# Kernel optimization log

Measured on AMD Instinct MI355X. Metric: run time of the kernel, lower is better.

The kernel has to match this reference:

```python
import jax, jax.numpy as jnp
import numpy as np

N_NODES = 50000


def _sage_conv(x, src, dst, Wl, bl, Wr):
    # PyG SAGEConv (mean aggr): out = lin_l(mean_{j in N(i)} x_j) + lin_r(x_i)
    msgs = x[src]                                              # [E, F]
    agg = jax.ops.segment_sum(msgs, dst, num_segments=N_NODES)  # [N, F]
    cnt = jax.ops.segment_sum(jnp.ones((dst.shape[0],), x.dtype), dst,
                              num_segments=N_NODES)
    mean = agg / jnp.maximum(cnt, 1.0)[:, None]
    return mean @ Wl + bl + x @ Wr


def setup_inputs() -> dict:
    key = jax.random.key(0)
    ks = jax.random.split(key, 12)
    in_c, hid_c, out_c = 128, 128, 64
    E, P = 800000, 200000
    s = lambda k, shp: jax.random.normal(k, shp, dtype=jnp.float32) * (1.0 / np.sqrt(shp[0]))
    return {
        "x": jax.random.normal(ks[0], (N_NODES, in_c), dtype=jnp.float32),
        "edge_index": jax.random.randint(ks[1], (2, E), 0, N_NODES),
        "edge_pairs": jax.random.randint(ks[2], (2, P), 0, N_NODES),
        "W1l": s(ks[3], (in_c, hid_c)),
        "b1": jnp.zeros((hid_c,), jnp.float32),
        "W1r": s(ks[4], (in_c, hid_c)),
        "W2l": s(ks[5], (hid_c, out_c)),
        "b2": jnp.zeros((out_c,), jnp.float32),
        "W2r": s(ks[6], (hid_c, out_c)),
        "Wlin": s(ks[7], (2 * out_c, 1)),
        "blin": jnp.zeros((1,), jnp.float32),
    }


def reference(x, edge_index, edge_pairs, W1l, b1, W1r, W2l, b2, W2r, Wlin, blin):
    src, dst = edge_index[0], edge_index[1]
    h = jax.nn.relu(_sage_conv(x, src, dst, W1l, b1, W1r))
    z = _sage_conv(h, src, dst, W2l, b2, W2r)                 # [N, out_c]
    ps, pd = edge_pairs[0], edge_pairs[1]
    hcat = jnp.concatenate([z[ps], z[pd]], axis=1)            # [P, 2*out_c]
    logits = hcat @ Wlin + blin                               # [P, 1]
    return jax.nn.sigmoid(logits).reshape(-1)
```

## Files before the change

### kernel.cpp

```cpp
#include <hip/hip_runtime.h>
#include <math.h>


typedef __attribute__((ext_vector_type(8))) short bf16x8;
typedef __attribute__((ext_vector_type(4))) float f32x4;
typedef unsigned int uint32;
typedef unsigned short ushort16;

#define MAXBUCK 784
#define NHB 512
#define SLABB 2048

__device__ __forceinline__ ushort16 f2bf(float f) {
    uint32 u = __float_as_uint(f);
    uint32 r = u + 0x7FFFu + ((u >> 16) & 1u);
    return (ushort16)(r >> 16);
}


__global__ __launch_bounds__(256)
void prep_kernel(const float* __restrict__ x, uint32* __restrict__ xh, long long n4,
                 const float* __restrict__ W1l, const float* __restrict__ W1r,
                 ushort16* __restrict__ W1t,
                 const float* __restrict__ W2l, const float* __restrict__ W2r,
                 const float* __restrict__ Wlin, const float* __restrict__ b2,
                 float* __restrict__ fw, float* __restrict__ fc,
                 const int* __restrict__ dst, int* __restrict__ hcnt, int E,
                 int nbx, int nbw1) {
    __shared__ int lh[MAXBUCK];
    int b = blockIdx.x;
    int t = threadIdx.x;
    if (b < nbx) {
        long long i = (long long)b * 256 + t;
        if (i < n4) {
            float4 v = ((const float4*)x)[i];
            uint2 o;
            o.x = (uint32)f2bf(v.x) | ((uint32)f2bf(v.y) << 16);
            o.y = (uint32)f2bf(v.z) | ((uint32)f2bf(v.w) << 16);
            ((uint2*)xh)[i] = o;
        }
    } else if (b < nbx + nbw1) {
        int idx = (b - nbx) * 256 + t;
        int n = idx >> 8, k = idx & 255;
        float v = (k < 128) ? W1l[k * 128 + n] : W1r[(k - 128) * 128 + n];
        W1t[idx ^ ((n & 7) << 3)] = f2bf(v);
    } else if (b == nbx + nbw1) {
        if (t < 128) {
            float a = 0.f, c = 0.f;
            for (int l = 0; l < 64; ++l) {
                float w = W2l[t * 64 + l];
                a += w * Wlin[l];
                c += w * Wlin[64 + l];
            }
            fw[t] = a; fw[128 + t] = c;
        } else {
            int k = t - 128;
            float a = 0.f, c = 0.f;
            for (int l = 0; l < 64; ++l) {
                float w = W2r[k * 64 + l];
                a += w * Wlin[l];
                c += w * Wlin[64 + l];
            }
            fw[256 + k] = a; fw[384 + k] = c;
        }
        if (t == 0) { float s = 0.f; for (int l = 0; l < 64; ++l) s += b2[l] * Wlin[l];      fc[0] = s; }
        if (t == 1) { float s = 0.f; for (int l = 0; l < 64; ++l) s += b2[l] * Wlin[64 + l]; fc[1] = s; }
    } else {
        int hb = b - nbx - nbw1 - 1;
        for (int i = t; i < MAXBUCK; i += 256) lh[i] = 0;
        __syncthreads();
        int per = (E + NHB - 1) / NHB;
        int e0 = hb * per, e1 = min(e0 + per, E);
        for (int e = e0 + t; e < e1; e += 256) atomicAdd(&lh[dst[e] >> 6], 1);
        __syncthreads();
        for (int i = t; i < MAXBUCK; i += 256)
            hcnt[hb * MAXBUCK + i] = lh[i];
    }
}


__global__ __launch_bounds__(256)
void offs_kernel(const int* __restrict__ hcnt, int* __restrict__ boff,
                 int* __restrict__ tot) {
    int k = blockIdx.x * 4 + (threadIdx.x >> 6);
    int lane = threadIdx.x & 63;
    if (k >= MAXBUCK) return;
    int carry = 0;
    #pragma unroll
    for (int c = 0; c < NHB / 64; ++c) {
        int hb = c * 64 + lane;
        int v = hcnt[hb * MAXBUCK + k];
        int s = v;
        #pragma unroll
        for (int off = 1; off < 64; off <<= 1) {
            int u = __shfl_up(s, off, 64);
            if (lane >= off) s += u;
        }
        boff[hb * MAXBUCK + k] = carry + s - v;
        carry += __shfl(s, 63, 64);
    }
    if (lane == 0) tot[k] = carry;
}


__global__ __launch_bounds__(256)
void scatter_kernel(const int* __restrict__ src, const int* __restrict__ dst,
                    const int* __restrict__ boff,
                    uint32* __restrict__ recs, int E) {
    __shared__ int lh[MAXBUCK];
    __shared__ int lb[MAXBUCK];
    int t = threadIdx.x;
    int hb = blockIdx.x;
    int per = (E + NHB - 1) / NHB;
    int e0 = hb * per, e1 = min(e0 + per, E);
    for (int i = t; i < MAXBUCK; i += 256) {
        lh[i] = 0;
        lb[i] = i * SLABB + boff[hb * MAXBUCK + i];
    }
    __syncthreads();
    for (int e = e0 + t; e < e1; e += 256) {
        int d = dst[e];
        int bk = d >> 6;
        int r = atomicAdd(&lh[bk], 1);
        int p = lb[bk] + r;
        if (p < (bk + 1) * SLABB)
            recs[p] = (uint32)src[e] | ((uint32)(d & 63) << 16);
    }
}


__global__ __launch_bounds__(1024)
void sortagg_kernel(const uint32* __restrict__ xh,
                    const uint32* __restrict__ recs, const int* __restrict__ tot,
                    int2* __restrict__ rowse, ushort16* __restrict__ esrc_g,
                    uint32* __restrict__ meanh, int N) {
    __shared__ int lh[64];
    __shared__ int st_[64];
    __shared__ unsigned short es[SLABB];
    int b = blockIdx.x;
    int t = threadIdx.x;
    int s0 = b * SLABB;
    int cntb = tot[b]; if (cntb > SLABB) cntb = SLABB;
    int s1 = s0 + cntb;
    if (t < 64) lh[t] = 0;
    __syncthreads();
    for (int i = s0 + t; i < s1; i += 1024)
        atomicAdd(&lh[recs[i] >> 16], 1);
    __syncthreads();
    if (t < 64) {
        int v = lh[t];
        int incl = v;
        #pragma unroll
        for (int off = 1; off < 64; off <<= 1) {
            int u = __shfl_up(incl, off, 64);
            if (t >= off) incl += u;
        }
        int excl = incl - v;
        int node = b * 64 + t;
        if (node < N) rowse[node] = make_int2(s0 + excl, v);
        st_[t] = excl;
        lh[t] = excl;
    }
    __syncthreads();
    for (int i = s0 + t; i < s1; i += 1024) {
        uint32 r = recs[i];
        int pos = atomicAdd(&lh[r >> 16], 1);
        unsigned short sv = (unsigned short)(r & 0xFFFFu);
        es[pos] = sv;
        ((unsigned short*)esrc_g)[s0 + pos] = sv;
    }
    __syncthreads();

    int wave = t >> 6, lane = t & 63;
    int q = lane >> 4;
    int w = lane & 15;
    for (int rr = 0; rr < 4; ++rr) {
        int n = wave * 4 + rr;
        int node = b * 64 + n;
        if (node >= N) break;
        int e0 = st_[n], e1 = lh[n];
        if (e0 == e1) {
            if (q == 0) ((uint4*)meanh)[(size_t)node * 16 + w] = make_uint4(0u, 0u, 0u, 0u);
            continue;
        }
        float acc[8] = {};
        for (int k = e0; k < e1; k += 16) {
            int idx[4]; float msk[4];
            #pragma unroll
            for (int j = 0; j < 4; ++j) {
                int e = k + q * 4 + j;
                int valid = e < e1;
                idx[j] = es[valid ? e : e0];
                msk[j] = valid ? 1.f : 0.f;
            }
            #pragma unroll
            for (int j = 0; j < 4; ++j) {
                uint4 v = ((const uint4*)xh)[(size_t)idx[j] * 16 + w];
                acc[0] += __uint_as_float(v.x << 16) * msk[j];
                acc[1] += __uint_as_float(v.x & 0xFFFF0000u) * msk[j];
                acc[2] += __uint_as_float(v.y << 16) * msk[j];
                acc[3] += __uint_as_float(v.y & 0xFFFF0000u) * msk[j];
                acc[4] += __uint_as_float(v.z << 16) * msk[j];
                acc[5] += __uint_as_float(v.z & 0xFFFF0000u) * msk[j];
                acc[6] += __uint_as_float(v.w << 16) * msk[j];
                acc[7] += __uint_as_float(v.w & 0xFFFF0000u) * msk[j];
            }
        }
        #pragma unroll
        for (int i = 0; i < 8; ++i) {
            acc[i] += __shfl_xor(acc[i], 16, 64);
            acc[i] += __shfl_xor(acc[i], 32, 64);
        }
        if (q == 0) {
            float inv = 1.0f / (float)(e1 - e0);
            uint4 o;
            o.x = (uint32)f2bf(acc[0] * inv) | ((uint32)f2bf(acc[1] * inv) << 16);
            o.y = (uint32)f2bf(acc[2] * inv) | ((uint32)f2bf(acc[3] * inv) << 16);
            o.z = (uint32)f2bf(acc[4] * inv) | ((uint32)f2bf(acc[5] * inv) << 16);
            o.w = (uint32)f2bf(acc[6] * inv) | ((uint32)f2bf(acc[7] * inv) << 16);
            ((uint4*)meanh)[(size_t)node * 16 + w] = o;
        }
    }
}


__global__ __launch_bounds__(256)
void gemm1_mfma_kernel(const ushort16* __restrict__ meanh,
                       const ushort16* __restrict__ xh,
                       const ushort16* __restrict__ W1t,
                       const float* __restrict__ b1,
                       const float* __restrict__ fw,
                       float2* __restrict__ pab, float2* __restrict__ quv, int N) {
    __shared__ uint4 w1s[4096];
    for (int u = threadIdx.x; u < 4096; u += 256)
        w1s[u] = ((const uint4*)W1t)[u];
    __syncthreads();
    int wave = threadIdx.x >> 6;
    int lane = threadIdx.x & 63;
    int m = lane & 15;
    int quad = lane >> 4;
    int row0 = blockIdx.x * 128 + wave * 32;
    int ar0 = row0 + m;      if (ar0 > N - 1) ar0 = N - 1;
    int ar1 = row0 + 16 + m; if (ar1 > N - 1) ar1 = N - 1;
    const char* wbase = (const char*)w1s;
    f32x4 acc[2][8];
    #pragma unroll
    for (int h = 0; h < 2; ++h)
        #pragma unroll
        for (int c = 0; c < 8; ++c) acc[h][c] = (f32x4){0.f, 0.f, 0.f, 0.f};
    #pragma unroll
    for (int ks = 0; ks < 8; ++ks) {
        int k0 = ks * 32;
        const ushort16* Ab = (ks < 4) ? meanh : xh;
        bf16x8 a0 = *(const bf16x8*)(Ab + (size_t)ar0 * 128 + (k0 & 127) + quad * 8);
        bf16x8 a1 = *(const bf16x8*)(Ab + (size_t)ar1 * 128 + (k0 & 127) + quad * 8);
        #pragma unroll
        for (int c = 0; c < 8; ++c) {
            int boff_ = (((c * 16 + m) << 9) + ((k0 + quad * 8) << 1)) ^ ((m & 7) << 4);
            bf16x8 bfr = *(const bf16x8*)(wbase + boff_);
            acc[0][c] = __builtin_amdgcn_mfma_f32_16x16x32_bf16(a0, bfr, acc[0][c], 0, 0, 0);
            acc[1][c] = __builtin_amdgcn_mfma_f32_16x16x32_bf16(a1, bfr, acc[1][c], 0, 0, 0);
        }
    }
    float da[2][4] = {}, dc[2][4] = {}, db[2][4] = {}, dd[2][4] = {};
    #pragma unroll
    for (int c = 0; c < 8; ++c) {
        int col = c * 16 + m;
        float bias = b1[col];
        float wa = fw[col], wc = fw[128 + col], wb = fw[256 + col], wd = fw[384 + col];
        #pragma unroll
        for (int h = 0; h < 2; ++h) {
            #pragma unroll
            for (int r = 0; r < 4; ++r) {
                float v = fmaxf(acc[h][c][r] + bias, 0.f);
                da[h][r] += v * wa; dc[h][r] += v * wc;
                db[h][r] += v * wb; dd[h][r] += v * wd;
            }
        }
    }
    #pragma unroll
    for (int h = 0; h < 2; ++h) {
        #pragma unroll
        for (int r = 0; r < 4; ++r) {
            #pragma unroll
            for (int msk = 1; msk < 16; msk <<= 1) {
                da[h][r] += __shfl_xor(da[h][r], msk, 64);
                dc[h][r] += __shfl_xor(dc[h][r], msk, 64);
                db[h][r] += __shfl_xor(db[h][r], msk, 64);
                dd[h][r] += __shfl_xor(dd[h][r], msk, 64);
            }
        }
    }
    if (m == 0) {
        #pragma unroll
        for (int h = 0; h < 2; ++h) {
            #pragma unroll
            for (int r = 0; r < 4; ++r) {
                int grow = row0 + h * 16 + quad * 4 + r;
                if (grow < N) {
                    pab[grow] = make_float2(da[h][r], dc[h][r]);
                    quv[grow] = make_float2(db[h][r], dd[h][r]);
                }
            }
        }
    }
}


__global__ __launch_bounds__(256)
void agg_link_kernel(const float2* __restrict__ pab,
                     const float2* __restrict__ quv,
                     const int2* __restrict__ rowse,
                     const ushort16* __restrict__ esrc,
                     const float* __restrict__ fc,
                     float* __restrict__ za, float* __restrict__ zb, int N) {
    int gi = blockIdx.x * blockDim.x + threadIdx.x;
    int i = gi >> 2;
    int q = gi & 3;
    if (i >= N) return;
    int2 se = rowse[i];
    int s0 = se.x, s1 = se.x + se.y;
    float a0 = 0.f, c0 = 0.f, a1 = 0.f, c1 = 0.f;
    for (int k = s0 + q; k < s1; k += 8) {
        int kB = k + 4;
        int vB = kB < s1;
        int idxA = esrc[k];
        int idxB = esrc[vB ? kB : k];
        float2 pA = pab[idxA];
        float2 pB = pab[idxB];
        float mB = vB ? 1.f : 0.f;
        a0 += pA.x; c0 += pA.y;
        a1 += pB.x * mB; c1 += pB.y * mB;
    }
    float spa = a0 + a1, spc = c0 + c1;
    spa += __shfl_xor(spa, 1, 64); spa += __shfl_xor(spa, 2, 64);
    spc += __shfl_xor(spc, 1, 64); spc += __shfl_xor(spc, 2, 64);
    if (q == 0) {
        float inv = (se.y > 0) ? 1.0f / (float)se.y : 0.f;
        float2 qv = quv[i];
        za[i] = spa * inv + qv.x + fc[0];
        zb[i] = spc * inv + qv.y + fc[1];
    }
}


__global__ void link_kernel(const float* __restrict__ za, const float* __restrict__ zb,
                            const int* __restrict__ ps, const int* __restrict__ pd,
                            const float* __restrict__ blin,
                            float* __restrict__ out, int P) {
    int p = blockIdx.x * blockDim.x + threadIdx.x;
    if (p >= P) return;
    float logit = za[ps[p]] + zb[pd[p]] + blin[0];
    out[p] = 1.0f / (1.0f + expf(-logit));
}


extern "C" void kernel_launch(void* const* d_in, const int* in_sizes, int n_in,
                              void* d_out, int out_size, void* d_ws, size_t ws_size,
                              hipStream_t stream) {
    const float* x          = (const float*)d_in[0];
    const int*   edge_index = (const int*)d_in[1];
    const int*   edge_pairs = (const int*)d_in[2];
    const float* W1l        = (const float*)d_in[3];
    const float* b1         = (const float*)d_in[4];
    const float* W1r        = (const float*)d_in[5];
    const float* W2l        = (const float*)d_in[6];
    const float* b2         = (const float*)d_in[7];
    const float* W2r        = (const float*)d_in[8];
    const float* Wlin       = (const float*)d_in[9];
    const float* blin       = (const float*)d_in[10];
    float* out = (float*)d_out;

    const int N = in_sizes[0] / 128;
    const int E = in_sizes[1] / 2;
    const int P = in_sizes[2] / 2;
    const int NBUCK = (N + 63) >> 6;

    const int* src = edge_index;
    const int* dst = edge_index + E;
    const int* ps  = edge_pairs;
    const int* pd  = edge_pairs + P;

    ushort16* xh    = (ushort16*)d_ws;
    ushort16* meanh = xh + (size_t)N * 128;
    ushort16* W1t   = meanh + (size_t)N * 128;
    float* fw      = (float*)(W1t + 128 * 256);
    float* fc      = fw + 512;
    float2* pab    = (float2*)(fc + 16);
    float2* quv    = pab + N;
    float* za      = (float*)(quv + N);
    float* zb      = za + N;
    int2* rowse    = (int2*)(zb + N);
    int* tot       = (int*)(rowse + N);
    int* hcnt      = tot + MAXBUCK;
    int* boff      = hcnt + NHB * MAXBUCK;
    uint32* recs   = (uint32*)(boff + NHB * MAXBUCK);
    ushort16* esrc = (ushort16*)(recs + (size_t)MAXBUCK * SLABB);

    const long long n4 = (long long)N * 128 / 4;
    const int nbx  = (int)((n4 + 255) / 256);
    const int nbw1 = 128;

    prep_kernel<<<nbx + nbw1 + 1 + NHB, 256, 0, stream>>>(
        x, (uint32*)xh, n4, W1l, W1r, W1t, W2l, W2r, Wlin, b2, fw, fc,
        dst, hcnt, E, nbx, nbw1);

    offs_kernel<<<MAXBUCK / 4, 256, 0, stream>>>(hcnt, boff, tot);
    scatter_kernel<<<NHB, 256, 0, stream>>>(src, dst, boff, recs, E);

    sortagg_kernel<<<NBUCK, 1024, 0, stream>>>((const uint32*)xh, recs, tot,
                                               rowse, esrc, (uint32*)meanh, N);

    gemm1_mfma_kernel<<<(N + 127) / 128, 256, 0, stream>>>(meanh, xh, W1t, b1, fw,
                                                           pab, quv, N);

    agg_link_kernel<<<(4 * N + 255) / 256, 256, 0, stream>>>(pab, quv, rowse, esrc, fc,
                                                             za, zb, N);

    link_kernel<<<(P + 255) / 256, 256, 0, stream>>>(za, zb, ps, pd, blin, out, P);
}
```

Baseline: 173.6 us.

## Stage scatter records in LDS and restructure per-node gather into paired half-row passes

The scatter kernel now uses fewer histogram blocks. Each block locally counting-sorts its edges by bucket in shared memory, then writes records to global memory in bucket-contiguous order, so global stores are more coalesced. The aggregation loop now processes two nodes at once per wave, splitting each 128-feature row into two 64-feature passes with 8 lanes per row and 8 edges in flight per node. This is meant to raise memory-level parallelism and balance work across nodes of different degree. In exchange it adds more shared memory, extra block-level prefix scans, fewer scatter blocks, and repeated es index reads across passes.

```diff
diff --git a/kernel.cpp b/kernel.cpp
--- a/kernel.cpp
+++ b/kernel.cpp
@@ -8,7 +8,8 @@
 typedef unsigned short ushort16;
 
 #define MAXBUCK 784
-#define NHB 512
+#define NHB 128
+#define SPB 6272
 #define SLABB 2048
 
 __device__ __forceinline__ ushort16 f2bf(float f) {
@@ -108,23 +109,58 @@
                     const int* __restrict__ boff,
                     uint32* __restrict__ recs, int E) {
     __shared__ int lh[MAXBUCK];
-    __shared__ int lb[MAXBUCK];
+    __shared__ int lstart[MAXBUCK];
+    __shared__ int lpart[256];
+    __shared__ uint32 stage[SPB];
+    __shared__ unsigned short bkid[SPB];
     int t = threadIdx.x;
     int hb = blockIdx.x;
     int per = (E + NHB - 1) / NHB;
     int e0 = hb * per, e1 = min(e0 + per, E);
-    for (int i = t; i < MAXBUCK; i += 256) {
-        lh[i] = 0;
-        lb[i] = i * SLABB + boff[hb * MAXBUCK + i];
-    }
+    for (int i = t; i < MAXBUCK; i += 256) lh[i] = 0;
+    __syncthreads();
+    for (int e = e0 + t; e < e1; e += 256) atomicAdd(&lh[dst[e] >> 6], 1);
+    __syncthreads();
+    int lo = t * 4;
+    int loc[4]; int s = 0;
+    #pragma unroll
+    for (int i2 = 0; i2 < 4; ++i2) {
+        int ix = lo + i2;
+        int v = (ix < MAXBUCK) ? lh[ix] : 0;
+        loc[i2] = v; s += v;
+    }
+    lpart[t] = s;
+    __syncthreads();
+    for (int off = 1; off < 256; off <<= 1) {
+        int v = (t >= off) ? lpart[t - off] : 0;
+        __syncthreads();
+        lpart[t] += v;
+        __syncthreads();
+    }
+    int run = (t == 0) ? 0 : lpart[t - 1];
+    #pragma unroll
+    for (int i2 = 0; i2 < 4; ++i2) {
+        int ix = lo + i2;
+        if (ix < MAXBUCK) lstart[ix] = run;
+        run += loc[i2];
+    }
+    __syncthreads();
+    for (int i = t; i < MAXBUCK; i += 256) lh[i] = lstart[i];
     __syncthreads();
     for (int e = e0 + t; e < e1; e += 256) {
         int d = dst[e];
         int bk = d >> 6;
-        int r = atomicAdd(&lh[bk], 1);
-        int p = lb[bk] + r;
-        if (p < (bk + 1) * SLABB)
-            recs[p] = (uint32)src[e] | ((uint32)(d & 63) << 16);
+        int p = atomicAdd(&lh[bk], 1);
+        stage[p] = (uint32)src[e] | ((uint32)(d & 63) << 16);
+        bkid[p] = (unsigned short)bk;
+    }
+    __syncthreads();
+    int nloc = e1 - e0;
+    for (int j = t; j < nloc; j += 256) {
+        int bk = bkid[j];
+        int gpos = bk * SLABB + boff[hb * MAXBUCK + bk] + (j - lstart[bk]);
+        if (gpos < (bk + 1) * SLABB)
+            recs[gpos] = stage[j];
     }
 }
 
@@ -172,53 +208,82 @@
     __syncthreads();
 
     int wave = t >> 6, lane = t & 63;
-    int q = lane >> 4;
-    int w = lane & 15;
-    for (int rr = 0; rr < 4; ++rr) {
-        int n = wave * 4 + rr;
-        int node = b * 64 + n;
-        if (node >= N) break;
-        int e0 = st_[n], e1 = lh[n];
-        if (e0 == e1) {
-            if (q == 0) ((uint4*)meanh)[(size_t)node * 16 + w] = make_uint4(0u, 0u, 0u, 0u);
-            continue;
-        }
-        float acc[8] = {};
-        for (int k = e0; k < e1; k += 16) {
-            int idx[4]; float msk[4];
+    int oct = lane >> 3;
+    int w = lane & 7;
+    for (int pass = 0; pass < 2; ++pass) {
+        for (int np = 0; np < 2; ++np) {
+            int nA = wave * 4 + np * 2, nB = nA + 1;
+            int nodeA = b * 64 + nA, nodeB = b * 64 + nB;
+            int e0A = st_[nA], e1A = lh[nA];
+            int e0B = st_[nB], e1B = lh[nB];
+            float accA[8] = {}, accB[8] = {};
+            int itA = (e1A - e0A + 15) >> 4;
+            int itB = (e1B - e0B + 15) >> 4;
+            int itn = itA > itB ? itA : itB;
+            int kA = e0A, kB = e0B;
+            for (int it = 0; it < itn; ++it) {
+                int idxA[2], idxB[2]; float mA[2], mB[2];
+                #pragma unroll
+                for (int j = 0; j < 2; ++j) {
+                    int eA = kA + j * 8 + oct;
+                    int vA = eA < e1A;
+                    idxA[j] = es[vA ? eA : 0];
+                    mA[j] = vA ? 1.f : 0.f;
+                    int eB = kB + j * 8 + oct;
+                    int vB = eB < e1B;
+                    idxB[j] = es[vB ? eB : 0];
+                    mB[j] = vB ? 1.f : 0.f;
+                }
+                #pragma unroll
+                for (int j = 0; j < 2; ++j) {
+                    uint4 v = ((const uint4*)xh)[(size_t)idxA[j] * 16 + pass * 8 + w];
+                    accA[0] += __uint_as_float(v.x << 16) * mA[j];
+                    accA[1] += __uint_as_float(v.x & 0xFFFF0000u) * mA[j];
+                    accA[2] += __uint_as_float(v.y << 16) * mA[j];
+                    accA[3] += __uint_as_float(v.y & 0xFFFF0000u) * mA[j];
+                    accA[4] += __uint_as_float(v.z << 16) * mA[j];
+                    accA[5] += __uint_as_float(v.z & 0xFFFF0000u) * mA[j];
+                    accA[6] += __uint_as_float(v.w << 16) * mA[j];
+                    accA[7] += __uint_as_float(v.w & 0xFFFF0000u) * mA[j];
+                    uint4 u = ((const uint4*)xh)[(size_t)idxB[j] * 16 + pass * 8 + w];
+                    accB[0] += __uint_as_float(u.x << 16) * mB[j];
+                    accB[1] += __uint_as_float(u.x & 0xFFFF0000u) * mB[j];
+                    accB[2] += __uint_as_float(u.y << 16) * mB[j];
+                    accB[3] += __uint_as_float(u.y & 0xFFFF0000u) * mB[j];
+                    accB[4] += __uint_as_float(u.z << 16) * mB[j];
+                    accB[5] += __uint_as_float(u.z & 0xFFFF0000u) * mB[j];
+                    accB[6] += __uint_as_float(u.w << 16) * mB[j];
+                    accB[7] += __uint_as_float(u.w & 0xFFFF0000u) * mB[j];
+                }
+                kA += 16; kB += 16;
+            }
             #pragma unroll
-            for (int j = 0; j < 4; ++j) {
-                int e = k + q * 4 + j;
-                int valid = e < e1;
-                idx[j] = es[valid ? e : e0];
-                msk[j] = valid ? 1.f : 0.f;
-            }
-            #pragma unroll
-            for (int j = 0; j < 4; ++j) {
-                uint4 v = ((const uint4*)xh)[(size_t)idx[j] * 16 + w];
-                acc[0] += __uint_as_float(v.x << 16) * msk[j];
-                acc[1] += __uint_as_float(v.x & 0xFFFF0000u) * msk[j];
-                acc[2] += __uint_as_float(v.y << 16) * msk[j];
-                acc[3] += __uint_as_float(v.y & 0xFFFF0000u) * msk[j];
-                acc[4] += __uint_as_float(v.z << 16) * msk[j];
-                acc[5] += __uint_as_float(v.z & 0xFFFF0000u) * msk[j];
-                acc[6] += __uint_as_float(v.w << 16) * msk[j];
-                acc[7] += __uint_as_float(v.w & 0xFFFF0000u) * msk[j];
-            }
-        }
-        #pragma unroll
-        for (int i = 0; i < 8; ++i) {
-            acc[i] += __shfl_xor(acc[i], 16, 64);
-            acc[i] += __shfl_xor(acc[i], 32, 64);
-        }
-        if (q == 0) {
-            float inv = 1.0f / (float)(e1 - e0);
-            uint4 o;
-            o.x = (uint32)f2bf(acc[0] * inv) | ((uint32)f2bf(acc[1] * inv) << 16);
-            o.y = (uint32)f2bf(acc[2] * inv) | ((uint32)f2bf(acc[3] * inv) << 16);
-            o.z = (uint32)f2bf(acc[4] * inv) | ((uint32)f2bf(acc[5] * inv) << 16);
-            o.w = (uint32)f2bf(acc[6] * inv) | ((uint32)f2bf(acc[7] * inv) << 16);
-            ((uint4*)meanh)[(size_t)node * 16 + w] = o;
+            for (int i = 0; i < 8; ++i) {
+                accA[i] += __shfl_xor(accA[i], 8, 64);
+                accA[i] += __shfl_xor(accA[i], 16, 64);
+                accA[i] += __shfl_xor(accA[i], 32, 64);
+                accB[i] += __shfl_xor(accB[i], 8, 64);
+                accB[i] += __shfl_xor(accB[i], 16, 64);
+                accB[i] += __shfl_xor(accB[i], 32, 64);
+            }
+            if (oct == 0 && nodeA < N) {
+                float inv = (e1A > e0A) ? 1.0f / (float)(e1A - e0A) : 0.f;
+                uint4 o;
+                o.x = (uint32)f2bf(accA[0] * inv) | ((uint32)f2bf(accA[1] * inv) << 16);
+                o.y = (uint32)f2bf(accA[2] * inv) | ((uint32)f2bf(accA[3] * inv) << 16);
+                o.z = (uint32)f2bf(accA[4] * inv) | ((uint32)f2bf(accA[5] * inv) << 16);
+                o.w = (uint32)f2bf(accA[6] * inv) | ((uint32)f2bf(accA[7] * inv) << 16);
+                ((uint4*)meanh)[(size_t)nodeA * 16 + pass * 8 + w] = o;
+            }
+            if (oct == 1 && nodeB < N) {
+                float inv = (e1B > e0B) ? 1.0f / (float)(e1B - e0B) : 0.f;
+                uint4 o;
+                o.x = (uint32)f2bf(accB[0] * inv) | ((uint32)f2bf(accB[1] * inv) << 16);
+                o.y = (uint32)f2bf(accB[2] * inv) | ((uint32)f2bf(accB[3] * inv) << 16);
+                o.z = (uint32)f2bf(accB[4] * inv) | ((uint32)f2bf(accB[5] * inv) << 16);
+                o.w = (uint32)f2bf(accB[6] * inv) | ((uint32)f2bf(accB[7] * inv) << 16);
+                ((uint4*)meanh)[(size_t)nodeB * 16 + pass * 8 + w] = o;
+            }
         }
     }
 }
```

Result: slower. 217.1 us (+25.1%).
